# Kernel optimization log

Measured on AMD Instinct MI355X. Metric: run time of the kernel, lower is better.

Reference implementation:

```python
import jax, jax.numpy as jnp
import numpy as np

N_NODES = 50000
N_EDGES = 800000
NODE_IN = 256
EDGE_OUT = 64
GLOBAL_IN = 128
NODE_OUT = 256
HIDDEN = 512
N_GRAPHS = 64


def setup_inputs() -> dict:
    key = jax.random.key(0)
    ks = jax.random.split(key, 8)
    x = jax.random.normal(ks[0], (N_NODES, NODE_IN), dtype=jnp.float32)
    edge_index = jax.random.randint(ks[1], (2, N_EDGES), 0, N_NODES, dtype=jnp.int64)
    edge_attr = jax.random.normal(ks[2], (N_EDGES, EDGE_OUT), dtype=jnp.float32)
    u = jax.random.normal(ks[3], (N_GRAPHS, GLOBAL_IN), dtype=jnp.float32)
    batch = jnp.sort(jax.random.randint(ks[4], (N_NODES,), 0, N_GRAPHS, dtype=jnp.int64))
    in_dim = NODE_IN + EDGE_OUT + GLOBAL_IN
    # MLP params (torch nn.Linear default init: U(-1/sqrt(fan_in), 1/sqrt(fan_in)))
    b1s = 1.0 / np.sqrt(in_dim)
    b2s = 1.0 / np.sqrt(HIDDEN)
    W1 = jax.random.uniform(ks[5], (in_dim, HIDDEN), dtype=jnp.float32, minval=-b1s, maxval=b1s)
    b1 = jnp.zeros((HIDDEN,), dtype=jnp.float32)
    W2 = jax.random.uniform(ks[6], (HIDDEN, NODE_OUT), dtype=jnp.float32, minval=-b2s, maxval=b2s)
    b2 = jnp.zeros((NODE_OUT,), dtype=jnp.float32)
    return {"x": x, "edge_index": edge_index, "edge_attr": edge_attr, "u": u,
            "batch": batch, "W1": W1, "b1": b1, "W2": W2, "b2": b2}


def reference(x, edge_index, edge_attr, u, batch, W1, b1, W2, b2):
    n = x.shape[0]
    src = edge_index[0]
    # scatter_mean(edge_attr, src, dim=0, dim_size=n)
    sums = jax.ops.segment_sum(edge_attr, src, num_segments=n)          # [N, E_out]
    counts = jax.ops.segment_sum(jnp.ones((edge_attr.shape[0],), edge_attr.dtype),
                                 src, num_segments=n)                   # [N]
    edge_attr_agg = sums / jnp.maximum(counts, 1.0)[:, None]
    u_expanded = u[batch]                                               # [N, G_in]
    combined = jnp.concatenate([x, edge_attr_agg, u_expanded], axis=1)  # [N, 448]
    h = jax.nn.relu(combined @ W1 + b1)                                 # [N, H]
    return h @ W2 + b2                                                  # [N, N_out]
```

## Files before the change

### kernel.cpp

```cpp
#include <hip/hip_runtime.h>
#include <hip/hip_bf16.h>
#include <stdint.h>

#define NN 50000
#define NE 800000
#define NODE_IN 256
#define EDGE_OUT 64
#define GLOBAL_IN 128
#define NODE_OUT 256
#define HIDDEN 512
#define IN_DIM 448
#define MAXDEG 64

typedef __attribute__((ext_vector_type(8))) short bf16x8;
typedef __attribute__((ext_vector_type(4))) float f32x4;
typedef __attribute__((ext_vector_type(4))) unsigned short us4;

__device__ __forceinline__ unsigned short f2bf(float x) {
    union { float f; unsigned int u; } c; c.f = x;
    unsigned int u = c.u;
    unsigned int r = (u + 0x7FFFu + ((u >> 16) & 1u)) >> 16;
    return (unsigned short)r;
}

#define GLD_LDS(gp, lp) __builtin_amdgcn_global_load_lds( \
    (const __attribute__((address_space(1))) unsigned int*)(gp), \
    (__attribute__((address_space(3))) unsigned int*)(lp), 16, 0, 0)

__global__ __launch_bounds__(256)
void fill_perm(const int* __restrict__ src, int* __restrict__ cnt,
               int* __restrict__ perm)
{
    int e = blockIdx.x * 256 + threadIdx.x;
    if (e < NE) {
        int s = src[e];
        int pos = atomicAdd(&cnt[s], 1);
        if (pos < MAXDEG) perm[(size_t)s * MAXDEG + pos] = e;
    }
}

__global__ __launch_bounds__(256)
void conv_w(const float* __restrict__ W1, const float* __restrict__ W2,
            unsigned short* __restrict__ W1T, unsigned short* __restrict__ W2T)
{
    int idx = blockIdx.x * 256 + threadIdx.x;
    if (idx < IN_DIM * HIDDEN) {
        int n = idx / IN_DIM, k = idx - n * IN_DIM;
        W1T[idx] = f2bf(W1[(size_t)k * HIDDEN + n]);
    } else {
        int j = idx - IN_DIM * HIDDEN;
        if (j < HIDDEN * NODE_OUT) {
            int n = j / HIDDEN, k = j - n * HIDDEN;
            W2T[j] = f2bf(W2[(size_t)k * NODE_OUT + n]);
        }
    }
}

__global__ __launch_bounds__(256)
void seg_comb(const float* __restrict__ edge_attr,
              const int* __restrict__ perm,
              const int* __restrict__ cnt,
              const float* __restrict__ x,
              const float* __restrict__ u,
              const int* __restrict__ batch,
              unsigned short* __restrict__ comb)
{
    int node = blockIdx.x * 4 + (threadIdx.x >> 6);
    if (node >= NN) return;
    int lane = threadIdx.x & 63;
    unsigned short* crow = comb + (size_t)node * IN_DIM;

    {
        const float4 v = *(const float4*)(x + (size_t)node * NODE_IN + lane * 4);
        us4 o = { f2bf(v.x), f2bf(v.y), f2bf(v.z), f2bf(v.w) };
        *(us4*)(crow + lane * 4) = o;
    }
    int b = batch[node];
    if (lane < 32) {
        const float4 v = *(const float4*)(u + (size_t)b * GLOBAL_IN + lane * 4);
        us4 o = { f2bf(v.x), f2bf(v.y), f2bf(v.z), f2bf(v.w) };
        *(us4*)(crow + NODE_IN + EDGE_OUT + lane * 4) = o;
    }
    int c = cnt[node];
    int cc = c < MAXDEG ? c : MAXDEG;
    int g = lane >> 4;
    int f = (lane & 15) * 4;
    const int* pbase = perm + (size_t)node * MAXDEG;
    float4 acc = make_float4(0.f, 0.f, 0.f, 0.f);
    for (int i = g; i < cc; i += 4) {
        int e = pbase[i];
        const float4 v = *(const float4*)(edge_attr + (size_t)e * EDGE_OUT + f);
        acc.x += v.x; acc.y += v.y; acc.z += v.z; acc.w += v.w;
    }
    #pragma unroll
    for (int off = 16; off < 64; off <<= 1) {
        acc.x += __shfl_xor(acc.x, off, 64);
        acc.y += __shfl_xor(acc.y, off, 64);
        acc.z += __shfl_xor(acc.z, off, 64);
        acc.w += __shfl_xor(acc.w, off, 64);
    }
    if (g == 0) {
        float inv = 1.0f / fmaxf((float)c, 1.0f);
        us4 o = { f2bf(acc.x * inv), f2bf(acc.y * inv),
                  f2bf(acc.z * inv), f2bf(acc.w * inv) };
        *(us4*)(crow + NODE_IN + f) = o;
    }
}

template<int EPI>
__global__ __launch_bounds__(256)
void gemm_bt_128(const unsigned short* __restrict__ A,
                 const unsigned short* __restrict__ B,
                 const float* __restrict__ bias,
                 void* __restrict__ Cv,
                 int M, int N, int K)
{
    __shared__ unsigned short lA[128 * 32];
    __shared__ unsigned short lB[128 * 32];
    const int tid = threadIdx.x;
    const int w = tid >> 6, l = tid & 63;
    const int m0 = blockIdx.y * 128;
    const int n0 = blockIdx.x * 128;
    const int wr = w >> 1, wc = w & 1;

    f32x4 acc[4][4] = {};

    const int cA0 = w * 64 + l;
    const int cA1 = (w + 4) * 64 + l;
    const int rA0 = cA0 >> 2, kA0 = (cA0 & 3) * 8;
    const int rA1 = cA1 >> 2, kA1 = (cA1 & 3) * 8;
    int gr0 = m0 + rA0; if (gr0 >= M) gr0 = M - 1;
    int gr1 = m0 + rA1; if (gr1 >= M) gr1 = M - 1;
    const unsigned short* pA0 = A + (size_t)gr0 * K + kA0;
    const unsigned short* pA1 = A + (size_t)gr1 * K + kA1;
    const unsigned short* pB0 = B + (size_t)(n0 + rA0) * K + kA0;
    const unsigned short* pB1 = B + (size_t)(n0 + rA1) * K + kA1;

    for (int k0 = 0; k0 < K; k0 += 32) {
        GLD_LDS(pA0 + k0, &lA[(size_t)cA0 * 8]);
        GLD_LDS(pA1 + k0, &lA[(size_t)cA1 * 8]);
        GLD_LDS(pB0 + k0, &lB[(size_t)cA0 * 8]);
        GLD_LDS(pB1 + k0, &lB[(size_t)cA1 * 8]);
        __syncthreads();

        bf16x8 af[4], bfr[4];
        #pragma unroll
        for (int m = 0; m < 4; ++m)
            af[m] = *(const bf16x8*)&lA[(wr * 64 + m * 16 + (l & 15)) * 32 + (l >> 4) * 8];
        #pragma unroll
        for (int n = 0; n < 4; ++n)
            bfr[n] = *(const bf16x8*)&lB[(wc * 64 + n * 16 + (l & 15)) * 32 + (l >> 4) * 8];

        #pragma unroll
        for (int m = 0; m < 4; ++m)
            #pragma unroll
            for (int n = 0; n < 4; ++n)
                acc[m][n] = __builtin_amdgcn_mfma_f32_16x16x32_bf16(af[m], bfr[n], acc[m][n], 0, 0, 0);

        __syncthreads();
    }

    const int cbase = n0 + wc * 64 + (l & 15);
    const int rbase = m0 + wr * 64 + ((l >> 4) << 2);
    if (EPI == 0) {
        unsigned short* C = (unsigned short*)Cv;
        #pragma unroll
        for (int m = 0; m < 4; ++m) {
            #pragma unroll
            for (int j = 0; j < 4; ++j) {
                int row = rbase + m * 16 + j;
                if (row < M) {
                    #pragma unroll
                    for (int n = 0; n < 4; ++n) {
                        int c = cbase + n * 16;
                        float v = acc[m][n][j] + bias[c];
                        v = fmaxf(v, 0.0f);
                        C[(size_t)row * N + c] = f2bf(v);
                    }
                }
            }
        }
    } else {
        float* C = (float*)Cv;
        #pragma unroll
        for (int m = 0; m < 4; ++m) {
            #pragma unroll
            for (int j = 0; j < 4; ++j) {
                int row = rbase + m * 16 + j;
                if (row < M) {
                    #pragma unroll
                    for (int n = 0; n < 4; ++n) {
                        int c = cbase + n * 16;
                        C[(size_t)row * N + c] = acc[m][n][j] + bias[c];
                    }
                }
            }
        }
    }
}

extern "C" void kernel_launch(void* const* d_in, const int* in_sizes, int n_in,
                              void* d_out, int out_size, void* d_ws, size_t ws_size,
                              hipStream_t stream)
{
    const float* x         = (const float*)d_in[0];
    const int*   edge_idx  = (const int*)d_in[1];
    const float* edge_attr = (const float*)d_in[2];
    const float* u         = (const float*)d_in[3];
    const int*   batch     = (const int*)d_in[4];
    const float* W1        = (const float*)d_in[5];
    const float* b1        = (const float*)d_in[6];
    const float* W2        = (const float*)d_in[7];
    const float* b2        = (const float*)d_in[8];
    float* out = (float*)d_out;

    char* ws = (char*)d_ws;
    int*            cnt    = (int*)(ws);
    int*            perm   = (int*)(ws + 200704);
    unsigned short* comb   = (unsigned short*)(ws + 13000704);
    unsigned short* W1T    = (unsigned short*)(ws + 57800704);
    unsigned short* W2T    = (unsigned short*)(ws + 58259456);
    unsigned short* h      = (unsigned short*)(ws + 58521600);

    hipMemsetAsync(cnt, 0, 200000, stream);

    fill_perm<<<(NE + 255) / 256, 256, 0, stream>>>(edge_idx, cnt, perm);

    conv_w<<<(IN_DIM * HIDDEN + HIDDEN * NODE_OUT + 255) / 256, 256, 0, stream>>>(
        W1, W2, W1T, W2T);

    seg_comb<<<(NN + 3) / 4, 256, 0, stream>>>(edge_attr, perm, cnt, x, u, batch, comb);

    gemm_bt_128<0><<<dim3(HIDDEN / 128, (NN + 127) / 128), 256, 0, stream>>>(
        comb, W1T, b1, h, NN, HIDDEN, IN_DIM);
    gemm_bt_128<1><<<dim3(NODE_OUT / 128, (NN + 127) / 128), 256, 0, stream>>>(
        h, W2T, b2, out, NN, NODE_OUT, HIDDEN);
}
```

Measured before the change: 220.4 us.

## Precompute per-graph u@W1 bias table and shrink first GEMM K to 320

The global-feature part of the first layer (u[batch] @ W1_u + b1) is computed once per graph (64x512) in a prep kernel. The GEMM epilogue adds the row's graph bias via a batch lookup, so the combined matrix and the first GEMM's K shrink from 448 to 320 columns. The cnt memset and weight conversion are merged into the same prep kernel, which removes one launch. The cost is an extra batch load and gathered bias load per row in the epilogue, plus the u-projection now being done in fp32.

```diff
diff --git a/kernel.cpp b/kernel.cpp
--- a/kernel.cpp
+++ b/kernel.cpp
@@ -9,7 +9,8 @@
 #define GLOBAL_IN 128
 #define NODE_OUT 256
 #define HIDDEN 512
-#define IN_DIM 448
+#define K1 320
+#define N_GRAPHS 64
 #define MAXDEG 64
 
 typedef __attribute__((ext_vector_type(8))) short bf16x8;
@@ -27,6 +28,38 @@
     (const __attribute__((address_space(1))) unsigned int*)(gp), \
     (__attribute__((address_space(3))) unsigned int*)(lp), 16, 0, 0)
 
+#define PREP_W1 (HIDDEN * K1)
+#define PREP_W2 (PREP_W1 + NODE_OUT * HIDDEN)
+#define PREP_G  (PREP_W2 + N_GRAPHS * HIDDEN)
+#define PREP_Z  (PREP_G + NN)
+__global__ __launch_bounds__(256)
+void prep(const float* __restrict__ W1, const float* __restrict__ W2,
+          const float* __restrict__ u, const float* __restrict__ b1,
+          unsigned short* __restrict__ W1T, unsigned short* __restrict__ W2T,
+          float* __restrict__ G, int* __restrict__ cnt)
+{
+    int idx = blockIdx.x * 256 + threadIdx.x;
+    if (idx < PREP_W1) {
+        int n = idx / K1, k = idx - n * K1;
+        W1T[idx] = f2bf(W1[(size_t)k * HIDDEN + n]);
+    } else if (idx < PREP_W2) {
+        int j = idx - PREP_W1;
+        int n = j / HIDDEN, k = j - n * HIDDEN;
+        W2T[j] = f2bf(W2[(size_t)k * NODE_OUT + n]);
+    } else if (idx < PREP_G) {
+        int j = idx - PREP_W2;
+        int g = j >> 9, col = j & 511;
+        const float* up = u + (size_t)g * GLOBAL_IN;
+        float acc = b1[col];
+        #pragma unroll 4
+        for (int k = 0; k < GLOBAL_IN; ++k)
+            acc += up[k] * W1[(size_t)(K1 + k) * HIDDEN + col];
+        G[j] = acc;
+    } else if (idx < PREP_Z) {
+        cnt[idx - PREP_G] = 0;
+    }
+}
+
 __global__ __launch_bounds__(256)
 void fill_perm(const int* __restrict__ src, int* __restrict__ cnt,
                int* __restrict__ perm)
@@ -40,46 +73,21 @@
 }
 
 __global__ __launch_bounds__(256)
-void conv_w(const float* __restrict__ W1, const float* __restrict__ W2,
-            unsigned short* __restrict__ W1T, unsigned short* __restrict__ W2T)
-{
-    int idx = blockIdx.x * 256 + threadIdx.x;
-    if (idx < IN_DIM * HIDDEN) {
-        int n = idx / IN_DIM, k = idx - n * IN_DIM;
-        W1T[idx] = f2bf(W1[(size_t)k * HIDDEN + n]);
-    } else {
-        int j = idx - IN_DIM * HIDDEN;
-        if (j < HIDDEN * NODE_OUT) {
-            int n = j / HIDDEN, k = j - n * HIDDEN;
-            W2T[j] = f2bf(W2[(size_t)k * NODE_OUT + n]);
-        }
-    }
-}
-
-__global__ __launch_bounds__(256)
 void seg_comb(const float* __restrict__ edge_attr,
               const int* __restrict__ perm,
               const int* __restrict__ cnt,
               const float* __restrict__ x,
-              const float* __restrict__ u,
-              const int* __restrict__ batch,
               unsigned short* __restrict__ comb)
 {
     int node = blockIdx.x * 4 + (threadIdx.x >> 6);
     if (node >= NN) return;
     int lane = threadIdx.x & 63;
-    unsigned short* crow = comb + (size_t)node * IN_DIM;
+    unsigned short* crow = comb + (size_t)node * K1;
 
     {
         const float4 v = *(const float4*)(x + (size_t)node * NODE_IN + lane * 4);
         us4 o = { f2bf(v.x), f2bf(v.y), f2bf(v.z), f2bf(v.w) };
         *(us4*)(crow + lane * 4) = o;
-    }
-    int b = batch[node];
-    if (lane < 32) {
-        const float4 v = *(const float4*)(u + (size_t)b * GLOBAL_IN + lane * 4);
-        us4 o = { f2bf(v.x), f2bf(v.y), f2bf(v.z), f2bf(v.w) };
-        *(us4*)(crow + NODE_IN + EDGE_OUT + lane * 4) = o;
     }
     int c = cnt[node];
     int cc = c < MAXDEG ? c : MAXDEG;
@@ -112,6 +120,7 @@
 void gemm_bt_128(const unsigned short* __restrict__ A,
                  const unsigned short* __restrict__ B,
                  const float* __restrict__ bias,
+                 const int* __restrict__ batch,
                  void* __restrict__ Cv,
                  int M, int N, int K)
 {
@@ -170,10 +179,11 @@
             for (int j = 0; j < 4; ++j) {
                 int row = rbase + m * 16 + j;
                 if (row < M) {
+                    const float* grow = bias + (size_t)batch[row] * HIDDEN;
                     #pragma unroll
                     for (int n = 0; n < 4; ++n) {
                         int c = cbase + n * 16;
-                        float v = acc[m][n][j] + bias[c];
+                        float v = acc[m][n][j] + grow[c];
                         v = fmaxf(v, 0.0f);
                         C[(size_t)row * N + c] = f2bf(v);
                     }
@@ -218,21 +228,19 @@
     int*            cnt    = (int*)(ws);
     int*            perm   = (int*)(ws + 200704);
     unsigned short* comb   = (unsigned short*)(ws + 13000704);
-    unsigned short* W1T    = (unsigned short*)(ws + 57800704);
-    unsigned short* W2T    = (unsigned short*)(ws + 58259456);
-    unsigned short* h      = (unsigned short*)(ws + 58521600);
-
-    hipMemsetAsync(cnt, 0, 200000, stream);
+    unsigned short* W1T    = (unsigned short*)(ws + 45000704);
+    unsigned short* W2T    = (unsigned short*)(ws + 45328384);
+    float*          G      = (float*)(ws + 45590528);
+    unsigned short* h      = (unsigned short*)(ws + 45721600);
+
+    prep<<<(PREP_Z + 255) / 256, 256, 0, stream>>>(W1, W2, u, b1, W1T, W2T, G, cnt);
 
     fill_perm<<<(NE + 255) / 256, 256, 0, stream>>>(edge_idx, cnt, perm);
 
-    conv_w<<<(IN_DIM * HIDDEN + HIDDEN * NODE_OUT + 255) / 256, 256, 0, stream>>>(
-        W1, W2, W1T, W2T);
-
-    seg_comb<<<(NN + 3) / 4, 256, 0, stream>>>(edge_attr, perm, cnt, x, u, batch, comb);
+    seg_comb<<<(NN + 3) / 4, 256, 0, stream>>>(edge_attr, perm, cnt, x, comb);
 
     gemm_bt_128<0><<<dim3(HIDDEN / 128, (NN + 127) / 128), 256, 0, stream>>>(
-        comb, W1T, b1, h, NN, HIDDEN, IN_DIM);
+        comb, W1T, G, batch, h, NN, HIDDEN, K1);
     gemm_bt_128<1><<<dim3(NODE_OUT / 128, (NN + 127) / 128), 256, 0, stream>>>(
-        h, W2T, b2, out, NN, NODE_OUT, HIDDEN);
-}
+        h, W2T, b2, nullptr, out, NN, NODE_OUT, HIDDEN);
+}
```

Measured after the change: 227.9 us. +3.4%, slower.
